# Kernel optimization log

Measured on AMD Instinct MI355X. Metric: run time of the kernel, lower is better.

## Reference

```python
import jax, jax.numpy as jnp
import numpy as np


def setup_inputs() -> dict:
    key = jax.random.key(0)
    ks = jax.random.split(key, 6)
    B, C, S, E = 8, 16, 512, 256
    wscale = (2.0 / (E + E)) ** 0.5  # xavier_normal for [E, E] fan_in=fan_out=E
    return {
        "query": jax.random.normal(ks[0], (B, C, S, E), dtype=jnp.float32),
        "key": jax.random.normal(ks[1], (B, C, S, E), dtype=jnp.float32),
        "value": jax.random.normal(ks[2], (B, C, S, E), dtype=jnp.float32),
        "q_proj_weight": jax.random.normal(ks[3], (C, E, E), dtype=jnp.float32) * wscale,
        "k_proj_weight": jax.random.normal(ks[4], (C, E, E), dtype=jnp.float32) * wscale,
        "v_proj_weight": jax.random.normal(ks[5], (C, E, E), dtype=jnp.float32) * wscale,
        "q_proj_bias": jnp.zeros((C, 1, E), dtype=jnp.float32),
        "k_proj_bias": jnp.zeros((C, 1, E), dtype=jnp.float32),
        "v_proj_bias": jnp.zeros((C, 1, E), dtype=jnp.float32),
    }


def reference(query, key, value, q_proj_weight, k_proj_weight, v_proj_weight,
              q_proj_bias, k_proj_bias, v_proj_bias):
    E = query.shape[-1]
    # Per-cycle projection + bias + ReLU.  b=batch, c=cycle, s/t=seq, e/f=embed
    q = jax.nn.relu(jnp.einsum("bcse,cef->bcsf", query, q_proj_weight) + q_proj_bias)
    k = jax.nn.relu(jnp.einsum("bcse,cef->bcsf", key, k_proj_weight) + k_proj_bias)
    v = jax.nn.relu(jnp.einsum("bcse,cef->bcsf", value, v_proj_weight) + v_proj_bias)
    q = q * (float(E) ** -0.5)
    attn = jax.nn.softmax(jnp.einsum("bcse,bcte->bcst", q, k), axis=-1)
    out = jnp.einsum("bcst,bcte->bcse", attn, v)
    return out
```

## Files before the change

### kernel.cpp

```cpp
#include <hip/hip_runtime.h>

constexpr int BATCH = 8;
constexpr int CYC   = 16;
constexpr int SEQ   = 512;
constexpr int EMB   = 256;

typedef __attribute__((ext_vector_type(8))) short bf16x8;
typedef __attribute__((ext_vector_type(4))) float f32x4;

__device__ __forceinline__ unsigned short f2bf(float x) {
    unsigned int u = __float_as_uint(x);
    u += 0x7fffu + ((u >> 16) & 1u);
    return (unsigned short)(u >> 16);
}
__device__ __forceinline__ unsigned int pk2(float lo, float hi) {
    return (unsigned int)f2bf(lo) | ((unsigned int)f2bf(hi) << 16);
}
__device__ __forceinline__ f32x4 mfma16(bf16x8 a, bf16x8 b, f32x4 c) {
    return __builtin_amdgcn_mfma_f32_16x16x32_bf16(a, b, c, 0, 0, 0);
}
__device__ __forceinline__ void gll16(const void* g, void* l) {
    __builtin_amdgcn_global_load_lds(
        (const __attribute__((address_space(1))) void*)g,
        (__attribute__((address_space(3))) void*)l, 16, 0, 0);
}

__global__ __launch_bounds__(256) void wt_kernel(const float* __restrict__ W,
                                                 unsigned short* __restrict__ Wt) {
    __shared__ float tile[64][65];
    const int c  = blockIdx.z;
    const int e0 = blockIdx.x * 64;
    const int f0 = blockIdx.y * 64;
    const float* Wc = W + (size_t)c * EMB * EMB;
    unsigned short* Wtc = Wt + (size_t)c * EMB * EMB;
    const int t = threadIdx.x;
    {
        const int er = t >> 4;
        const int fc = (t & 15) * 4;
        for (int i = 0; i < 4; ++i) {
            const float4 v = *(const float4*)(Wc + (size_t)(e0 + er + i * 16) * EMB + f0 + fc);
            tile[er + i * 16][fc + 0] = v.x;
            tile[er + i * 16][fc + 1] = v.y;
            tile[er + i * 16][fc + 2] = v.z;
            tile[er + i * 16][fc + 3] = v.w;
        }
    }
    __syncthreads();
    {
        const int fr = t >> 4;
        const int ec = (t & 15) * 4;
        for (int i = 0; i < 4; ++i) {
            const int f = fr + i * 16;
            ushort4 o;
            o.x = f2bf(tile[ec + 0][f]);
            o.y = f2bf(tile[ec + 1][f]);
            o.z = f2bf(tile[ec + 2][f]);
            o.w = f2bf(tile[ec + 3][f]);
            *(ushort4*)(Wtc + (size_t)(f0 + f) * EMB + e0 + ec) = o;
        }
    }
}

__global__ __launch_bounds__(256, 4) void proj_kernel(
    const float* __restrict__ Xq, const float* __restrict__ Xk,
    const float* __restrict__ Xv,
    const unsigned short* __restrict__ Wq, const unsigned short* __restrict__ Wk,
    const unsigned short* __restrict__ Wv,
    const float* __restrict__ Bq, const float* __restrict__ Bk,
    const float* __restrict__ Bv,
    unsigned short* __restrict__ Yq, unsigned short* __restrict__ Yk,
    unsigned short* __restrict__ Yv)
{
    __shared__ unsigned short As[2][64 * 32];
    __shared__ unsigned short Bs[2][256 * 32];

    const int z = blockIdx.z;
    const float* X = z == 0 ? Xq : z == 1 ? Xk : Xv;
    const unsigned short* Wt = z == 0 ? Wq : z == 1 ? Wk : Wv;
    const float* bias = z == 0 ? Bq : z == 1 ? Bk : Bv;
    unsigned short* Y = z == 0 ? Yq : z == 1 ? Yk : Yv;
    const float scale = z == 0 ? 0.0625f : 1.0f;

    const int bc = blockIdx.x;
    const int c  = bc & (CYC - 1);
    const int m0 = blockIdx.y * 64;
    const float* Xb = X + (size_t)bc * SEQ * EMB;
    const unsigned short* Wc = Wt + (size_t)c * EMB * EMB;
    const float* bb = bias + (size_t)c * EMB;
    unsigned short* Yb = Y + (size_t)bc * SEQ * EMB;

    const int tid  = threadIdx.x;
    const int lane = tid & 63, w = tid >> 6;
    const int ln   = lane & 15, quad = lane >> 4;
    const int wu   = __builtin_amdgcn_readfirstlane(w);

    const int ar = tid >> 2, ac = (tid & 3) * 8;
    const int brow = lane >> 2;
    const int gch  = (lane & 3) ^ ((lane >> 3) & 3);
    const int bslot = quad ^ ((ln >> 1) & 3);

    f32x4 acc[4][4];
    for (int i = 0; i < 4; ++i)
        for (int j = 0; j < 4; ++j) acc[i][j] = (f32x4){0.f, 0.f, 0.f, 0.f};

    const float* aptr = Xb + (size_t)(m0 + ar) * EMB + ac;
    float4 a0, a1;

    auto aload = [&](int kk) {
        const float* p = aptr + kk * 32;
        a0 = *(const float4*)p;
        a1 = *(const float4*)(p + 4);
    };
    auto bstage = [&](int kk, int b) {
        const int k0 = kk * 32;
#pragma unroll
        for (int j = 0; j < 4; ++j) {
            const int r0 = wu * 64 + j * 16;
            gll16(Wc + (size_t)(r0 + brow) * EMB + k0 + gch * 8,
                  &Bs[b][r0 * 32]);
        }
    };

    aload(0);
    __builtin_amdgcn_sched_barrier(0);
    bstage(0, 0);

#pragma unroll
    for (int kk = 0; kk < 8; ++kk) {
        const int cur = kk & 1;
        asm volatile("s_waitcnt vmcnt(4)" ::: "memory");
        {
            int4 pk;
            pk.x = pk2(a0.x, a0.y); pk.y = pk2(a0.z, a0.w);
            pk.z = pk2(a1.x, a1.y); pk.w = pk2(a1.z, a1.w);
            *(int4*)&As[cur][ar * 32 + ac] = pk;
        }
        if (kk < 7) {
            aload(kk + 1);
            __builtin_amdgcn_sched_barrier(0);
            bstage(kk + 1, cur ^ 1);
            asm volatile("s_waitcnt vmcnt(6)" ::: "memory");
        } else {
            asm volatile("s_waitcnt vmcnt(0)" ::: "memory");
        }
        asm volatile("s_waitcnt lgkmcnt(0)" ::: "memory");
        __builtin_amdgcn_s_barrier();
        __builtin_amdgcn_sched_barrier(0);

        bf16x8 af[4], bfv[4];
#pragma unroll
        for (int i = 0; i < 4; ++i)
            af[i] = *(const bf16x8*)&As[cur][(i * 16 + ln) * 32 + quad * 8];
#pragma unroll
        for (int j = 0; j < 4; ++j)
            bfv[j] = *(const bf16x8*)&Bs[cur][(w * 64 + j * 16 + ln) * 32 + bslot * 8];
#pragma unroll
        for (int i = 0; i < 4; ++i)
#pragma unroll
            for (int j = 0; j < 4; ++j)
                acc[i][j] = mfma16(af[i], bfv[j], acc[i][j]);

        __builtin_amdgcn_sched_barrier(0);
        asm volatile("s_waitcnt lgkmcnt(0)" ::: "memory");
        __builtin_amdgcn_s_barrier();
    }

    float bvj[4];
#pragma unroll
    for (int j = 0; j < 4; ++j) bvj[j] = bb[w * 64 + j * 16 + ln];

    if (z != 2) {
        unsigned short* ep = &Bs[0][0] + w * 1152;
        for (int i = 0; i < 4; ++i) {
            for (int j = 0; j < 4; ++j)
                for (int r = 0; r < 4; ++r)
                    ep[(quad * 4 + r) * 72 + j * 16 + ln] =
                        f2bf(fmaxf(acc[i][j][r] + bvj[j], 0.f) * scale);
            __syncthreads();
            for (int h = 0; h < 2; ++h) {
                const int cid = lane + h * 64;
                const int row = cid >> 3, ch = cid & 7;
                *(bf16x8*)&Yb[(size_t)(m0 + i * 16 + row) * EMB + w * 64 + ch * 8] =
                    *(const bf16x8*)&ep[row * 72 + ch * 8];
            }
            __syncthreads();
        }
    } else {
        for (int j = 0; j < 4; ++j) {
            const int fg = w * 64 + j * 16 + ln;
            for (int i = 0; i < 4; ++i) {
                const int mb = m0 + i * 16 + quad * 4;
                ushort4 u;
                u.x = f2bf(fmaxf(acc[i][j][0] + bvj[j], 0.f) * scale);
                u.y = f2bf(fmaxf(acc[i][j][1] + bvj[j], 0.f) * scale);
                u.z = f2bf(fmaxf(acc[i][j][2] + bvj[j], 0.f) * scale);
                u.w = f2bf(fmaxf(acc[i][j][3] + bvj[j], 0.f) * scale);
                *(ushort4*)&Yb[(size_t)fg * SEQ + mb] = u;
            }
        }
    }
}

__global__ __launch_bounds__(256) void attn_kernel(
    const unsigned short* __restrict__ Qp, const unsigned short* __restrict__ Kp,
    const unsigned short* __restrict__ Vt, float* __restrict__ Out)
{
    __shared__ unsigned short Ks[32][264];
    __shared__ unsigned short Vs[256][40];
    __shared__ unsigned short Ps[64][40];
    const int bc = blockIdx.x;
    const int qt = blockIdx.y;
    const unsigned short* Qb = Qp + (size_t)bc * SEQ * EMB;
    const unsigned short* Kb = Kp + (size_t)bc * SEQ * EMB;
    const unsigned short* Vb = Vt + (size_t)bc * SEQ * EMB;
    float* Ob = Out + (size_t)bc * SEQ * EMB;

    const int tid  = threadIdx.x;
    const int lane = tid & 63, w = tid >> 6;
    const int ln   = lane & 15, quad = lane >> 4;

    bf16x8 qf[8];
    const int qrow = qt * 64 + w * 16 + ln;
    for (int ke = 0; ke < 8; ++ke)
        qf[ke] = *(const bf16x8*)(Qb + (size_t)qrow * EMB + ke * 32 + quad * 8);

    f32x4 of[16];
    for (int n = 0; n < 16; ++n) of[n] = (f32x4){0.f, 0.f, 0.f, 0.f};
    float lsum[4] = {0.f, 0.f, 0.f, 0.f};

    for (int tt = 0; tt < 16; ++tt) {
        const int t0 = tt * 32;
        for (int i = 0; i < 4; ++i) {
            const int idx = tid + i * 256;
            const int r = idx >> 5, c8 = (idx & 31) * 8;
            *(bf16x8*)&Ks[r][c8] = *(const bf16x8*)(Kb + (size_t)(t0 + r) * EMB + c8);
        }
        for (int i = 0; i < 4; ++i) {
            const int idx = tid + i * 256;
            const int e = idx >> 2, c8 = (idx & 3) * 8;
            *(bf16x8*)&Vs[e][c8] = *(const bf16x8*)(Vb + (size_t)e * SEQ + t0 + c8);
        }
        __syncthreads();

        f32x4 sf0 = (f32x4){0.f,0.f,0.f,0.f}, sf1 = (f32x4){0.f,0.f,0.f,0.f};
        for (int ke = 0; ke < 8; ++ke) {
            bf16x8 b0 = *(const bf16x8*)&Ks[ln][ke * 32 + quad * 8];
            bf16x8 b1 = *(const bf16x8*)&Ks[16 + ln][ke * 32 + quad * 8];
            sf0 = mfma16(qf[ke], b0, sf0);
            sf1 = mfma16(qf[ke], b1, sf1);
        }

        float p0[4], p1[4];
        for (int r = 0; r < 4; ++r) {
            p0[r] = __expf(sf0[r]);
            p1[r] = __expf(sf1[r]);
            lsum[r] += p0[r] + p1[r];
        }
        for (int r = 0; r < 4; ++r) {
            Ps[w * 16 + quad * 4 + r][ln]      = f2bf(p0[r]);
            Ps[w * 16 + quad * 4 + r][16 + ln] = f2bf(p1[r]);
        }
        __syncthreads();

        bf16x8 af = *(const bf16x8*)&Ps[w * 16 + ln][quad * 8];
        for (int n = 0; n < 16; ++n) {
            bf16x8 bv = *(const bf16x8*)&Vs[n * 16 + ln][quad * 8];
            of[n] = mfma16(af, bv, of[n]);
        }
        __syncthreads();
    }

    for (int off = 1; off < 16; off <<= 1)
        for (int r = 0; r < 4; ++r)
            lsum[r] += __shfl_xor(lsum[r], off, 64);
    float inv[4];
    for (int r = 0; r < 4; ++r) inv[r] = 1.0f / lsum[r];
    const int mbase = qt * 64 + w * 16 + quad * 4;
    for (int n = 0; n < 16; ++n)
        for (int r = 0; r < 4; ++r)
            Ob[(size_t)(mbase + r) * EMB + n * 16 + ln] = of[n][r] * inv[r];
}

extern "C" void kernel_launch(void* const* d_in, const int* in_sizes, int n_in,
                              void* d_out, int out_size, void* d_ws, size_t ws_size,
                              hipStream_t stream) {
    const float* query = (const float*)d_in[0];
    const float* key_  = (const float*)d_in[1];
    const float* value = (const float*)d_in[2];
    const float* wq = (const float*)d_in[3];
    const float* wk = (const float*)d_in[4];
    const float* wv = (const float*)d_in[5];
    const float* bq = (const float*)d_in[6];
    const float* bk = (const float*)d_in[7];
    const float* bv = (const float*)d_in[8];
    float* out = (float*)d_out;

    char* ws = (char*)d_ws;
    const size_t wsz = (size_t)CYC * EMB * EMB * sizeof(unsigned short);
    const size_t psz = (size_t)BATCH * CYC * SEQ * EMB * sizeof(unsigned short);
    unsigned short* Wtq = (unsigned short*)(ws);
    unsigned short* Wtk = (unsigned short*)(ws + wsz);
    unsigned short* Wtv = (unsigned short*)(ws + 2 * wsz);
    unsigned short* Qp  = (unsigned short*)(ws + 3 * wsz);
    unsigned short* Kp  = (unsigned short*)(ws + 3 * wsz + psz);
    unsigned short* Vtp = (unsigned short*)(ws + 3 * wsz + 2 * psz);

    const dim3 tb(256);
    wt_kernel<<<dim3(4, 4, CYC), tb, 0, stream>>>(wq, Wtq);
    wt_kernel<<<dim3(4, 4, CYC), tb, 0, stream>>>(wk, Wtk);
    wt_kernel<<<dim3(4, 4, CYC), tb, 0, stream>>>(wv, Wtv);

    proj_kernel<<<dim3(BATCH * CYC, SEQ / 64, 3), tb, 0, stream>>>(
        query, key_, value, Wtq, Wtk, Wtv, bq, bk, bv, Qp, Kp, Vtp);

    attn_kernel<<<dim3(BATCH * CYC, SEQ / 64), tb, 0, stream>>>(Qp, Kp, Vtp, out);
}
```

Baseline: 338.2 us.

## Restructure projection pipeline and stage transposed V output through LDS

```diff
diff --git a/kernel.cpp b/kernel.cpp
--- a/kernel.cpp
+++ b/kernel.cpp
@@ -71,8 +71,7 @@
     unsigned short* __restrict__ Yq, unsigned short* __restrict__ Yk,
     unsigned short* __restrict__ Yv)
 {
-    __shared__ unsigned short As[2][64 * 32];
-    __shared__ unsigned short Bs[2][256 * 32];
+    __shared__ unsigned short smem[20480];
 
     const int z = blockIdx.z;
     const float* X = z == 0 ? Xq : z == 1 ? Xk : Xv;
@@ -104,56 +103,65 @@
         for (int j = 0; j < 4; ++j) acc[i][j] = (f32x4){0.f, 0.f, 0.f, 0.f};
 
     const float* aptr = Xb + (size_t)(m0 + ar) * EMB + ac;
-    float4 a0, a1;
-
-    auto aload = [&](int kk) {
+    float4 av[2][2];
+
+    auto aload = [&](int kk, float4* dst) {
         const float* p = aptr + kk * 32;
-        a0 = *(const float4*)p;
-        a1 = *(const float4*)(p + 4);
+        dst[0] = *(const float4*)p;
+        dst[1] = *(const float4*)(p + 4);
     };
     auto bstage = [&](int kk, int b) {
         const int k0 = kk * 32;
+        unsigned short* Bb = smem + 4096 + b * 8192;
 #pragma unroll
         for (int j = 0; j < 4; ++j) {
             const int r0 = wu * 64 + j * 16;
             gll16(Wc + (size_t)(r0 + brow) * EMB + k0 + gch * 8,
-                  &Bs[b][r0 * 32]);
+                  Bb + (size_t)r0 * 32);
         }
     };
 
-    aload(0);
+    aload(0, av[0]);
     __builtin_amdgcn_sched_barrier(0);
     bstage(0, 0);
 
 #pragma unroll
     for (int kk = 0; kk < 8; ++kk) {
         const int cur = kk & 1;
-        asm volatile("s_waitcnt vmcnt(4)" ::: "memory");
+        unsigned short* As = smem + cur * 2048;
+        unsigned short* Bs = smem + 4096 + cur * 8192;
+
+        if (kk < 7) {
+            aload(kk + 1, av[cur ^ 1]);
+            asm volatile("s_waitcnt vmcnt(6)" ::: "memory");
+        } else {
+            asm volatile("s_waitcnt vmcnt(4)" ::: "memory");
+        }
         {
             int4 pk;
-            pk.x = pk2(a0.x, a0.y); pk.y = pk2(a0.z, a0.w);
-            pk.z = pk2(a1.x, a1.y); pk.w = pk2(a1.z, a1.w);
-            *(int4*)&As[cur][ar * 32 + ac] = pk;
+            pk.x = pk2(av[cur][0].x, av[cur][0].y);
+            pk.y = pk2(av[cur][0].z, av[cur][0].w);
+            pk.z = pk2(av[cur][1].x, av[cur][1].y);
+            pk.w = pk2(av[cur][1].z, av[cur][1].w);
+            *(int4*)&As[ar * 32 + ac] = pk;
         }
         if (kk < 7) {
-            aload(kk + 1);
-            __builtin_amdgcn_sched_barrier(0);
-            bstage(kk + 1, cur ^ 1);
-            asm volatile("s_waitcnt vmcnt(6)" ::: "memory");
+            asm volatile("s_waitcnt vmcnt(2)" ::: "memory");
         } else {
             asm volatile("s_waitcnt vmcnt(0)" ::: "memory");
         }
         asm volatile("s_waitcnt lgkmcnt(0)" ::: "memory");
         __builtin_amdgcn_s_barrier();
         __builtin_amdgcn_sched_barrier(0);
+        if (kk < 7) bstage(kk + 1, cur ^ 1);
 
         bf16x8 af[4], bfv[4];
 #pragma unroll
         for (int i = 0; i < 4; ++i)
-            af[i] = *(const bf16x8*)&As[cur][(i * 16 + ln) * 32 + quad * 8];
+            af[i] = *(const bf16x8*)&As[(i * 16 + ln) * 32 + quad * 8];
 #pragma unroll
         for (int j = 0; j < 4; ++j)
-            bfv[j] = *(const bf16x8*)&Bs[cur][(w * 64 + j * 16 + ln) * 32 + bslot * 8];
+            bfv[j] = *(const bf16x8*)&Bs[(w * 64 + j * 16 + ln) * 32 + bslot * 8];
 #pragma unroll
         for (int i = 0; i < 4; ++i)
 #pragma unroll
@@ -162,41 +170,46 @@
 
         __builtin_amdgcn_sched_barrier(0);
         asm volatile("s_waitcnt lgkmcnt(0)" ::: "memory");
-        __builtin_amdgcn_s_barrier();
-    }
+    }
+    __syncthreads();
 
     float bvj[4];
 #pragma unroll
     for (int j = 0; j < 4; ++j) bvj[j] = bb[w * 64 + j * 16 + ln];
 
     if (z != 2) {
-        unsigned short* ep = &Bs[0][0] + w * 1152;
+        unsigned short* ep = smem + w * 1152;
         for (int i = 0; i < 4; ++i) {
             for (int j = 0; j < 4; ++j)
                 for (int r = 0; r < 4; ++r)
                     ep[(quad * 4 + r) * 72 + j * 16 + ln] =
                         f2bf(fmaxf(acc[i][j][r] + bvj[j], 0.f) * scale);
-            __syncthreads();
             for (int h = 0; h < 2; ++h) {
                 const int cid = lane + h * 64;
                 const int row = cid >> 3, ch = cid & 7;
                 *(bf16x8*)&Yb[(size_t)(m0 + i * 16 + row) * EMB + w * 64 + ch * 8] =
                     *(const bf16x8*)&ep[row * 72 + ch * 8];
             }
-            __syncthreads();
         }
     } else {
+        unsigned short* ep = smem + w * 4864;
         for (int j = 0; j < 4; ++j) {
-            const int fg = w * 64 + j * 16 + ln;
+            const int fr = j * 16 + ln;
             for (int i = 0; i < 4; ++i) {
-                const int mb = m0 + i * 16 + quad * 4;
                 ushort4 u;
                 u.x = f2bf(fmaxf(acc[i][j][0] + bvj[j], 0.f) * scale);
                 u.y = f2bf(fmaxf(acc[i][j][1] + bvj[j], 0.f) * scale);
                 u.z = f2bf(fmaxf(acc[i][j][2] + bvj[j], 0.f) * scale);
                 u.w = f2bf(fmaxf(acc[i][j][3] + bvj[j], 0.f) * scale);
-                *(ushort4*)&Yb[(size_t)fg * SEQ + mb] = u;
+                *(ushort4*)&ep[fr * 76 + i * 16 + quad * 4] = u;
             }
+        }
+        const int fg0 = w * 64;
+        for (int h = 0; h < 8; ++h) {
+            const int cid = lane + h * 64;
+            const int row = cid >> 3, ch = cid & 7;
+            *(bf16x8*)&Yb[(size_t)(fg0 + row) * SEQ + m0 + ch * 8] =
+                *(const bf16x8*)&ep[row * 76 + ch * 8];
         }
     }
 }
```

Result: no change. 333.4 us (-1.4%).
